# Kernel optimization log

Measured on AMD Instinct MI355X. Metric: run time of the kernel, lower is better.

The kernel has to match this reference:

```python
import jax, jax.numpy as jnp
import numpy as np

B, N, M, C1, C2 = 4, 8192, 2048, 128, 256
H1, H2 = 256, 128  # mlp = [C2+C1, 256, 128]
EPS_DIST = 1e-8
EPS_BN = 1e-5
K = 3


def setup_inputs() -> dict:
    key = jax.random.key(0)
    ks = jax.random.split(key, 6)
    return {
        "unknown": jax.random.normal(ks[0], (B, N, 3), dtype=jnp.float32),
        "known": jax.random.normal(ks[1], (B, M, 3), dtype=jnp.float32),
        "unknow_feats": jax.random.normal(ks[2], (B, C1, N), dtype=jnp.float32),
        "known_feats": jax.random.normal(ks[3], (B, C2, M), dtype=jnp.float32),
        "W1": jax.random.normal(ks[4], (H1, C1 + C2), dtype=jnp.float32) * 0.05,
        "g1": jnp.ones((H1,), jnp.float32),
        "b1": jnp.zeros((H1,), jnp.float32),
        "W2": jax.random.normal(ks[5], (H2, H1), dtype=jnp.float32) * 0.05,
        "g2": jnp.ones((H2,), jnp.float32),
        "b2": jnp.zeros((H2,), jnp.float32),
    }


def _bn_relu(x, g, b):
    # training-mode BatchNorm over (batch, spatial) axes for (B, C, N) tensor
    mean = jnp.mean(x, axis=(0, 2), keepdims=True)
    var = jnp.var(x, axis=(0, 2), keepdims=True)
    y = (x - mean) * jax.lax.rsqrt(var + EPS_BN) * g[None, :, None] + b[None, :, None]
    return jax.nn.relu(y)


def reference(unknown, known, unknow_feats, known_feats, W1, g1, b1, W2, g2, b2):
    # 3-NN: squared euclidean distances (B, N, M) via expansion (avoids B,N,M,3 temp)
    d2 = (
        jnp.sum(unknown * unknown, axis=-1)[:, :, None]
        + jnp.sum(known * known, axis=-1)[:, None, :]
        - 2.0 * jnp.einsum("bnc,bmc->bnm", unknown, known)
    )
    neg_d, idx = jax.lax.top_k(-d2, K)  # smallest-K squared dists
    dist = -neg_d  # (B, N, K), squared distances (pytorch3d knn_points convention)
    recip = 1.0 / (dist + EPS_DIST)
    weight = recip / jnp.sum(recip, axis=2, keepdims=True)  # (B, N, K)

    kf = jnp.swapaxes(known_feats, 1, 2)  # (B, M, C2)
    grouped = jax.vmap(lambda f, i: f[i])(kf, idx)  # (B, N, K, C2)
    interp = jnp.einsum("bnkc,bnk->bcn", grouped, weight)  # (B, C2, N)

    x = jnp.concatenate([interp, unknow_feats], axis=1)  # (B, C2+C1, N)
    x = _bn_relu(jnp.einsum("oc,bcn->bon", W1, x), g1, b1)
    x = _bn_relu(jnp.einsum("oc,bcn->bon", W2, x), g2, b2)
    return x  # (B, H2, N)
```

## Files before the change

### kernel.cpp

```cpp
#include <hip/hip_runtime.h>
#include <hip/hip_bf16.h>
#include <cstdint>
#include <cstddef>

typedef unsigned short u16;
typedef __attribute__((ext_vector_type(8))) short bf16x8;
typedef __attribute__((ext_vector_type(4))) float f32x4;

constexpr int Bn = 4;
constexpr int Nq = 8192;
constexpr int Mk = 2048;
constexpr int C1c = 128;
constexpr int C2c = 256;
constexpr int H1c = 256;
constexpr int H2c = 128;

__device__ __forceinline__ float bf2f(u16 u) {
    union { uint32_t i; float f; } v;
    v.i = (uint32_t)u << 16;
    return v.f;
}
__device__ __forceinline__ u16 f2bf(float f) {
    const uint32_t x = __float_as_uint(f);
    return (u16)((x + 0x7FFFu + ((x >> 16) & 1u)) >> 16);
}
__device__ __forceinline__ uint32_t cvtpk(float lo, float hi) {
    uint32_t r;
    asm("v_cvt_pk_bf16_f32 %0, %1, %2" : "=v"(r) : "v"(lo), "v"(hi));
    return r;
}

__global__ __launch_bounds__(256) void knn_prep_kernel(
    const float* __restrict__ W1, const float* __restrict__ W2,
    u16* __restrict__ W1b, u16* __restrict__ W2b,
    const float* __restrict__ KF, u16* __restrict__ Ptb,
    const float* __restrict__ UF, u16* __restrict__ UFt,
    const float* __restrict__ unknown, const float* __restrict__ known,
    int* __restrict__ idx_out, float* __restrict__ w_out)
{
    __shared__ __align__(16) char smem[32768];
    const int bid = blockIdx.x;
    const int t = threadIdx.x;

    if (bid < 1024) {
        float4* kp = (float4*)smem;
        const int b = bid >> 8;
        const int n0 = (bid & 255) * 32;

        const float* kb = known + (size_t)b * Mk * 3;
        for (int i = t; i < Mk; i += 256) {
            const float x = kb[i * 3 + 0], y = kb[i * 3 + 1], z = kb[i * 3 + 2];
            kp[i] = make_float4(x, y, z, fmaf(x, x, fmaf(y, y, z * z)));
        }
        __syncthreads();

        const int q = n0 + (t >> 3);
        const int s = t & 7;
        const float* u = unknown + ((size_t)b * Nq + q) * 3;
        const float ux = u[0], uy = u[1], uz = u[2];
        const float nux = -2.0f * ux, nuy = -2.0f * uy, nuz = -2.0f * uz;
        const float uu = fmaf(ux, ux, fmaf(uy, uy, uz * uz));

        float d0 = 1e30f, d1 = 1e30f, d2 = 1e30f;
        int i0 = 0, i1 = 0, i2 = 0;

        auto ins = [&](float d, int i) {
            const bool c0 = d < d0, c1 = d < d1, c2 = d < d2;
            const float nd0 = fminf(d0, d);
            const float nd1 = __builtin_amdgcn_fmed3f(d0, d, d1);
            const float nd2 = __builtin_amdgcn_fmed3f(d1, d, d2);
            i2 = c1 ? i1 : (c2 ? i : i2);
            i1 = c0 ? i0 : (c1 ? i : i1);
            i0 = c0 ? i : i0;
            d0 = nd0; d1 = nd1; d2 = nd2;
        };

        #pragma unroll 8
        for (int it = 0; it < Mk / 8; ++it) {
            const int m = it * 8 + s;
            const float4 p = kp[m];
            const float d = fmaf(nux, p.x, fmaf(nuy, p.y, fmaf(nuz, p.z, p.w)));
            ins(d, m);
        }
        #pragma unroll
        for (int off = 1; off <= 4; off <<= 1) {
            const float e0 = __shfl_xor(d0, off), e1 = __shfl_xor(d1, off), e2 = __shfl_xor(d2, off);
            const int j0 = __shfl_xor(i0, off), j1 = __shfl_xor(i1, off), j2 = __shfl_xor(i2, off);
            ins(e0, j0);
            ins(e1, j1);
            ins(e2, j2);
        }
        if (s == 0) {
            const float f0 = d0 + uu, f1 = d1 + uu, f2 = d2 + uu;
            const float r0 = 1.0f / (f0 + 1e-8f);
            const float r1 = 1.0f / (f1 + 1e-8f);
            const float r2 = 1.0f / (f2 + 1e-8f);
            const float inv = 1.0f / (r0 + r1 + r2);
            const size_t base = ((size_t)b * Nq + q) * 3;
            idx_out[base + 0] = i0;
            idx_out[base + 1] = i1;
            idx_out[base + 2] = i2;
            w_out[base + 0] = r0 * inv;
            w_out[base + 1] = r1 * inv;
            w_out[base + 2] = r2 * inv;
        }
    } else if (bid < 1152) {
        const int cb = bid - 1024;
        const float* X = (cb < 96) ? W1 : W2;
        u16* Y = (cb < 96) ? W1b : W2b;
        const int i = ((cb < 96) ? cb : (cb - 96)) * 256 + t;
        const float4 v = *(const float4*)&X[(size_t)i * 4];
        ushort4 o;
        o.x = f2bf(v.x); o.y = f2bf(v.y); o.z = f2bf(v.z); o.w = f2bf(v.w);
        *(ushort4*)&Y[(size_t)i * 4] = o;
    } else if (bid < 1664) {
        u16* As = (u16*)smem;
        u16* Bs = (u16*)(smem + 5120);
        const int f = bid - 1152;
        const int b = f >> 7;
        const int rem = f & 127;
        const int m0 = (rem >> 2) * 64;
        const int h0 = (rem & 3) * 64;
        const float* KFb = KF + (size_t)b * C2c * Mk;
        const int l = t & 63, wv = t >> 6;
        const int wr = wv >> 1, wc = wv & 1;

        f32x4 acc[2][2];
        const f32x4 z = {0.0f, 0.0f, 0.0f, 0.0f};
        acc[0][0] = z; acc[0][1] = z; acc[1][0] = z; acc[1][1] = z;

        const int cA = t >> 3;
        const int mcA = (t & 7) * 8;
        const int hB = t >> 2;
        const int khB = (t & 3) * 8;

        for (int kt = 0; kt < 8; ++kt) {
            const int kc = kt * 32;
            {
                const float* src = &KFb[(size_t)(kc + cA) * Mk + m0 + mcA];
                const float4 v0 = *(const float4*)&src[0];
                const float4 v1 = *(const float4*)&src[4];
                As[(mcA + 0) * 40 + cA] = f2bf(v0.x);
                As[(mcA + 1) * 40 + cA] = f2bf(v0.y);
                As[(mcA + 2) * 40 + cA] = f2bf(v0.z);
                As[(mcA + 3) * 40 + cA] = f2bf(v0.w);
                As[(mcA + 4) * 40 + cA] = f2bf(v1.x);
                As[(mcA + 5) * 40 + cA] = f2bf(v1.y);
                As[(mcA + 6) * 40 + cA] = f2bf(v1.z);
                As[(mcA + 7) * 40 + cA] = f2bf(v1.w);
            }
            {
                const float* src = &W1[(size_t)(h0 + hB) * 384 + kc + khB];
                const float4 v0 = *(const float4*)&src[0];
                const float4 v1 = *(const float4*)&src[4];
                u16 o[8] = {f2bf(v0.x), f2bf(v0.y), f2bf(v0.z), f2bf(v0.w),
                            f2bf(v1.x), f2bf(v1.y), f2bf(v1.z), f2bf(v1.w)};
                *(uint4*)&Bs[hB * 40 + khB] = *(const uint4*)o;
            }
            __syncthreads();
            bf16x8 af[2], bf[2];
            #pragma unroll
            for (int ff = 0; ff < 2; ++ff) {
                af[ff] = *(const bf16x8*)&As[(wr * 32 + ff * 16 + (l & 15)) * 40 + (l >> 4) * 8];
                bf[ff] = *(const bf16x8*)&Bs[(wc * 32 + ff * 16 + (l & 15)) * 40 + (l >> 4) * 8];
            }
            #pragma unroll
            for (int i = 0; i < 2; ++i)
                #pragma unroll
                for (int j = 0; j < 2; ++j)
                    acc[i][j] = __builtin_amdgcn_mfma_f32_16x16x32_bf16(af[i], bf[j], acc[i][j], 0, 0, 0);
            __syncthreads();
        }

        u16* Pb = Ptb + (size_t)b * Mk * 256;
        const int cb = l & 15, rg = (l >> 4) * 4;
        #pragma unroll
        for (int i = 0; i < 2; ++i) {
            #pragma unroll
            for (int r = 0; r < 4; ++r) {
                const int row = m0 + wr * 32 + i * 16 + rg + r;
                #pragma unroll
                for (int j = 0; j < 2; ++j)
                    Pb[(size_t)row * 256 + h0 + wc * 32 + j * 16 + cb] = f2bf(acc[i][j][r]);
            }
        }
    } else {
        const int f = bid - 1664;
        const int b = f >> 8, rem = f & 255;
        const int m0 = (rem >> 1) * 64, c0 = (rem & 1) * 64;
        const float* X = UF + (size_t)b * C1c * Nq;
        u16* Y = UFt + (size_t)b * Nq * C1c;
        float (*T)[65] = (float(*)[65])smem;
        const int m4 = (t & 15) * 4, cr = t >> 4;
        #pragma unroll
        for (int i = 0; i < 4; ++i) {
            const float4 v = *(const float4*)&X[(size_t)(c0 + cr + i * 16) * Nq + m0 + m4];
            T[cr + i * 16][m4 + 0] = v.x;
            T[cr + i * 16][m4 + 1] = v.y;
            T[cr + i * 16][m4 + 2] = v.z;
            T[cr + i * 16][m4 + 3] = v.w;
        }
        __syncthreads();
        const int c4 = (t & 15) * 4, mr = t >> 4;
        #pragma unroll
        for (int i = 0; i < 4; ++i) {
            const int m = mr + i * 16;
            ushort4 o;
            o.x = f2bf(T[c4 + 0][m]);
            o.y = f2bf(T[c4 + 1][m]);
            o.z = f2bf(T[c4 + 2][m]);
            o.w = f2bf(T[c4 + 3][m]);
            *(ushort4*)&Y[(size_t)(m0 + m) * C1c + c0 + c4] = o;
        }
    }
}

__global__ __launch_bounds__(256) void mfma_gemm2(
    const u16* __restrict__ A,
    const u16* __restrict__ Bt,
    u16* __restrict__ Cout,
    const u16* __restrict__ Ptb,
    const int* __restrict__ idx, const float* __restrict__ wgt,
    float* __restrict__ partS, float* __restrict__ partQ)
{
    __shared__ __align__(16) char smem[16384];
    __shared__ float redS[4][128], redQ[4][128];
    u16* As = (u16*)smem;
    u16* Bs = (u16*)(smem + 8192);
    float (*Ytmp)[128] = (float(*)[128])smem;

    const int b = blockIdx.z;
    const int m0 = blockIdx.x * 128, n0 = blockIdx.y * 128;
    const int t = threadIdx.x;
    const int l = t & 63, wv = t >> 6;
    const int wr = wv >> 1, wc = wv & 1;

    const u16* Ab = A + (size_t)b * Nq * C1c;
    const int rA0 = t >> 2, rA1 = (t + 256) >> 2;
    const int ko = (t & 3) * 8;

    f32x4 acc[4][4];
    const f32x4 z = {0.0f, 0.0f, 0.0f, 0.0f};
    #pragma unroll
    for (int i = 0; i < 4; ++i)
        #pragma unroll
        for (int j = 0; j < 4; ++j) acc[i][j] = z;

    uint4 a0 = *(const uint4*)&Ab[(size_t)(m0 + rA0) * C1c + ko];
    uint4 a1 = *(const uint4*)&Ab[(size_t)(m0 + rA1) * C1c + ko];
    uint4 b0 = *(const uint4*)&Bt[(size_t)(n0 + rA0) * 384 + ko];
    uint4 b1 = *(const uint4*)&Bt[(size_t)(n0 + rA1) * 384 + ko];

    for (int kt = 0; kt < C1c / 32; ++kt) {
        *(uint4*)&As[t * 8] = a0;
        *(uint4*)&As[(t + 256) * 8] = a1;
        *(uint4*)&Bs[t * 8] = b0;
        *(uint4*)&Bs[(t + 256) * 8] = b1;
        __syncthreads();
        if (kt + 1 < C1c / 32) {
            const int k0 = (kt + 1) * 32;
            a0 = *(const uint4*)&Ab[(size_t)(m0 + rA0) * C1c + k0 + ko];
            a1 = *(const uint4*)&Ab[(size_t)(m0 + rA1) * C1c + k0 + ko];
            b0 = *(const uint4*)&Bt[(size_t)(n0 + rA0) * 384 + k0 + ko];
            b1 = *(const uint4*)&Bt[(size_t)(n0 + rA1) * 384 + k0 + ko];
        }
        bf16x8 af[4], bf[4];
        #pragma unroll
        for (int f = 0; f < 4; ++f) {
            af[f] = *(const bf16x8*)&As[(wr * 64 + f * 16 + (l & 15)) * 32 + (l >> 4) * 8];
            bf[f] = *(const bf16x8*)&Bs[(wc * 64 + f * 16 + (l & 15)) * 32 + (l >> 4) * 8];
        }
        #pragma unroll
        for (int i = 0; i < 4; ++i)
            #pragma unroll
            for (int j = 0; j < 4; ++j)
                acc[i][j] = __builtin_amdgcn_mfma_f32_16x16x32_bf16(af[i], bf[j], acc[i][j], 0, 0, 0);
        __syncthreads();
    }

    const int cb = l & 15;
    const int rg = (l >> 4) * 4;
    const int colblk = t & 15;
    const int rowblk = t >> 4;
    float s8[8] = {0, 0, 0, 0, 0, 0, 0, 0}, q8[8] = {0, 0, 0, 0, 0, 0, 0, 0};
    const u16* Pb = Ptb + (size_t)b * Mk * 256;

    for (int q = 0; q < 4; ++q) {
        __syncthreads();
        if (wr == (q >> 1)) {
            #pragma unroll
            for (int ii = 0; ii < 2; ++ii) {
                const int i = (q & 1) * 2 + ii;
                #pragma unroll
                for (int r = 0; r < 4; ++r) {
                    const int Rq = ii * 16 + rg + r;
                    #pragma unroll
                    for (int j = 0; j < 4; ++j)
                        Ytmp[Rq][wc * 64 + j * 16 + cb] = acc[i][j][r];
                }
            }
        }
        __syncthreads();
        #pragma unroll
        for (int rr = 0; rr < 2; ++rr) {
            const int Rq = rowblk * 2 + rr;
            const int R = m0 + q * 32 + Rq;
            const size_t ib = ((size_t)b * Nq + R) * 3;
            const int j0 = idx[ib], j1 = idx[ib + 1], j2 = idx[ib + 2];
            const float w0 = wgt[ib], w1 = wgt[ib + 1], w2 = wgt[ib + 2];
            const int c8 = colblk * 8;
            const int Cc0 = n0 + c8;
            const float* yrow = &Ytmp[Rq][c8];
            const float4 y0 = *(const float4*)&yrow[0];
            const float4 y1v = *(const float4*)&yrow[4];
            const uint4 p0 = *(const uint4*)&Pb[(size_t)j0 * 256 + Cc0];
            const uint4 p1 = *(const uint4*)&Pb[(size_t)j1 * 256 + Cc0];
            const uint4 p2 = *(const uint4*)&Pb[(size_t)j2 * 256 + Cc0];
            const u16* pp0 = (const u16*)&p0;
            const u16* pp1 = (const u16*)&p1;
            const u16* pp2 = (const u16*)&p2;
            const float* ya = (const float*)&y0;
            const float* yb = (const float*)&y1v;
            float v[8];
            #pragma unroll
            for (int c = 0; c < 8; ++c) {
                const float a = (c < 4) ? ya[c] : yb[c - 4];
                const float vv = a + w0 * bf2f(pp0[c]) + w1 * bf2f(pp1[c]) + w2 * bf2f(pp2[c]);
                v[c] = vv;
                s8[c] += vv;
                q8[c] += vv * vv;
            }
            uint4 o;
            uint32_t* po = (uint32_t*)&o;
            po[0] = cvtpk(v[0], v[1]);
            po[1] = cvtpk(v[2], v[3]);
            po[2] = cvtpk(v[4], v[5]);
            po[3] = cvtpk(v[6], v[7]);
            *(uint4*)&Cout[(size_t)b * Nq * 256 + (size_t)R * 256 + Cc0] = o;
        }
    }

    #pragma unroll
    for (int c = 0; c < 8; ++c) {
        s8[c] += __shfl_xor(s8[c], 16);
        s8[c] += __shfl_xor(s8[c], 32);
        q8[c] += __shfl_xor(q8[c], 16);
        q8[c] += __shfl_xor(q8[c], 32);
    }
    if (l < 16) {
        #pragma unroll
        for (int c = 0; c < 8; ++c) {
            redS[wv][l * 8 + c] = s8[c];
            redQ[wv][l * 8 + c] = q8[c];
        }
    }
    __syncthreads();
    if (t < 128) {
        const float S = redS[0][t] + redS[1][t] + redS[2][t] + redS[3][t];
        const float Q = redQ[0][t] + redQ[1][t] + redQ[2][t] + redQ[3][t];
        const int pblk = blockIdx.z * gridDim.x + blockIdx.x;
        partS[(size_t)pblk * 256 + blockIdx.y * 128 + t] = S;
        partQ[(size_t)pblk * 256 + blockIdx.y * 128 + t] = Q;
    }
}

__global__ __launch_bounds__(256) void bn1_finalize_mb(
    const float* __restrict__ pS, const float* __restrict__ pQ,
    const float* __restrict__ g, const float* __restrict__ beta,
    float* __restrict__ scale, float* __restrict__ bias)
{
    __shared__ float rs[256], rq[256];
    const int cc = threadIdx.x & 15;
    const int sl = threadIdx.x >> 4;
    const int ch = blockIdx.x * 16 + cc;
    float s = 0.0f, q = 0.0f;
    for (int i = sl; i < 256; i += 16) {
        s += pS[(size_t)i * 256 + ch];
        q += pQ[(size_t)i * 256 + ch];
    }
    rs[threadIdx.x] = s;
    rq[threadIdx.x] = q;
    __syncthreads();
    if (sl == 0) {
        for (int k = 1; k < 16; ++k) {
            s += rs[k * 16 + cc];
            q += rq[k * 16 + cc];
        }
        const float cnt = (float)(Bn * Nq);
        const float mean = s / cnt;
        const float var = q / cnt - mean * mean;
        const float rv = rsqrtf(var + 1e-5f);
        const float sc = g[ch] * rv;
        scale[ch] = sc;
        bias[ch] = beta[ch] - mean * sc;
    }
}

__device__ __forceinline__ uint4 bnx(uint4 x, const float* scs, const float* bis, int k) {
    const u16* p = (const u16*)&x;
    const float4 s0 = *(const float4*)&scs[k];
    const float4 s1 = *(const float4*)&scs[k + 4];
    const float4 b0 = *(const float4*)&bis[k];
    const float4 b1 = *(const float4*)&bis[k + 4];
    const float* sa = (const float*)&s0;
    const float* sb = (const float*)&s1;
    const float* ba = (const float*)&b0;
    const float* bb = (const float*)&b1;
    uint4 o;
    uint32_t* po = (uint32_t*)&o;
    #pragma unroll
    for (int w2 = 0; w2 < 2; ++w2) {
        const float a0 = fmaxf(0.0f, fmaf(bf2f(p[2 * w2 + 0]), sa[2 * w2 + 0], ba[2 * w2 + 0]));
        const float a1 = fmaxf(0.0f, fmaf(bf2f(p[2 * w2 + 1]), sa[2 * w2 + 1], ba[2 * w2 + 1]));
        po[w2] = cvtpk(a0, a1);
    }
    #pragma unroll
    for (int w2 = 0; w2 < 2; ++w2) {
        const float a0 = fmaxf(0.0f, fmaf(bf2f(p[4 + 2 * w2 + 0]), sb[2 * w2 + 0], bb[2 * w2 + 0]));
        const float a1 = fmaxf(0.0f, fmaf(bf2f(p[4 + 2 * w2 + 1]), sb[2 * w2 + 1], bb[2 * w2 + 1]));
        po[2 + w2] = cvtpk(a0, a1);
    }
    return o;
}

__global__ __launch_bounds__(256) void mfma_gemm3(
    const u16* __restrict__ W2b,
    const u16* __restrict__ Y,
    float* __restrict__ out,
    const float* __restrict__ bn_s, const float* __restrict__ bn_b,
    float* __restrict__ partS, float* __restrict__ partQ)
{
    __shared__ u16 As[2048];
    __shared__ u16 Bs[4096];
    __shared__ float scs[256], bis[256];
    __shared__ float sS[2][64], sQ[2][64];

    const int b = blockIdx.z;
    const int m0 = blockIdx.x * 64;
    const int n0 = blockIdx.y * 128;
    const int t = threadIdx.x;
    const int l = t & 63, wv = t >> 6;
    const int wr = wv >> 1, wc = wv & 1;

    scs[t] = bn_s[t];
    bis[t] = bn_b[t];

    const u16* Yb = Y + (size_t)b * Nq * 256;
    const int rA = t >> 2;
    const int rB1 = (t + 256) >> 2;
    const int ko = (t & 3) * 8;

    f32x4 acc[2][4];
    const f32x4 z = {0.0f, 0.0f, 0.0f, 0.0f};
    #pragma unroll
    for (int i = 0; i < 2; ++i)
        #pragma unroll
        for (int j = 0; j < 4; ++j) acc[i][j] = z;

    uint4 a0 = *(const uint4*)&W2b[(size_t)(m0 + rA) * 256 + ko];
    uint4 b0 = *(const uint4*)&Yb[(size_t)(n0 + rA) * 256 + ko];
    uint4 b1 = *(const uint4*)&Yb[(size_t)(n0 + rB1) * 256 + ko];
    __syncthreads();

    for (int kt = 0; kt < 8; ++kt) {
        const int k = kt * 32 + ko;
        *(uint4*)&As[t * 8] = a0;
        *(uint4*)&Bs[t * 8] = bnx(b0, scs, bis, k);
        *(uint4*)&Bs[(t + 256) * 8] = bnx(b1, scs, bis, k);
        __syncthreads();
        if (kt + 1 < 8) {
            const int k0 = (kt + 1) * 32;
            a0 = *(const uint4*)&W2b[(size_t)(m0 + rA) * 256 + k0 + ko];
            b0 = *(const uint4*)&Yb[(size_t)(n0 + rA) * 256 + k0 + ko];
            b1 = *(const uint4*)&Yb[(size_t)(n0 + rB1) * 256 + k0 + ko];
        }
        bf16x8 af[2], bf[4];
        #pragma unroll
        for (int f = 0; f < 2; ++f)
            af[f] = *(const bf16x8*)&As[(wr * 32 + f * 16 + (l & 15)) * 32 + (l >> 4) * 8];
        #pragma unroll
        for (int f = 0; f < 4; ++f)
            bf[f] = *(const bf16x8*)&Bs[(wc * 64 + f * 16 + (l & 15)) * 32 + (l >> 4) * 8];
        #pragma unroll
        for (int i = 0; i < 2; ++i)
            #pragma unroll
            for (int j = 0; j < 4; ++j)
                acc[i][j] = __builtin_amdgcn_mfma_f32_16x16x32_bf16(af[i], bf[j], acc[i][j], 0, 0, 0);
        __syncthreads();
    }

    const int cb = l & 15;
    const int rg = (l >> 4) * 4;
    float* ob = out + (size_t)b * H2c * Nq;
    #pragma unroll
    for (int i = 0; i < 2; ++i) {
        #pragma unroll
        for (int r = 0; r < 4; ++r) {
            const int Rl = wr * 32 + i * 16 + rg + r;
            #pragma unroll
            for (int j = 0; j < 4; ++j) {
                const int Cc = n0 + wc * 64 + j * 16 + cb;
                ob[(size_t)(m0 + Rl) * Nq + Cc] = acc[i][j][r];
            }
            float s = acc[i][0][r] + acc[i][1][r] + acc[i][2][r] + acc[i][3][r];
            float q = acc[i][0][r] * acc[i][0][r] + acc[i][1][r] * acc[i][1][r] +
                      acc[i][2][r] * acc[i][2][r] + acc[i][3][r] * acc[i][3][r];
            s += __shfl_xor(s, 1); s += __shfl_xor(s, 2);
            s += __shfl_xor(s, 4); s += __shfl_xor(s, 8);
            q += __shfl_xor(q, 1); q += __shfl_xor(q, 2);
            q += __shfl_xor(q, 4); q += __shfl_xor(q, 8);
            if ((l & 15) == 0) {
                sS[wc][Rl] = s;
                sQ[wc][Rl] = q;
            }
        }
    }
    __syncthreads();
    if (t < 64) {
        const float S = sS[0][t] + sS[1][t];
        const float Q = sQ[0][t] + sQ[1][t];
        const int p = blockIdx.z * gridDim.y + blockIdx.y;
        partS[(size_t)p * 128 + m0 + t] = S;
        partQ[(size_t)p * 128 + m0 + t] = Q;
    }
}

__global__ __launch_bounds__(256) void bn2_apply_kernel(
    float* __restrict__ Y,
    const float* __restrict__ pS, const float* __restrict__ pQ,
    const float* __restrict__ g, const float* __restrict__ beta)
{
    __shared__ float rs[256], rq[256];
    const int t = threadIdx.x;
    const size_t base = (size_t)blockIdx.x * 1024;
    const int c = (int)((base / Nq) % H2c);

    rs[t] = pS[(size_t)t * 128 + c];
    rq[t] = pQ[(size_t)t * 128 + c];
    __syncthreads();
    for (int off = 128; off > 0; off >>= 1) {
        if (t < off) {
            rs[t] += rs[t + off];
            rq[t] += rq[t + off];
        }
        __syncthreads();
    }
    if (t == 0) {
        const float cnt = (float)(Bn * Nq);
        const float mean = rs[0] / cnt;
        const float var = rq[0] / cnt - mean * mean;
        const float r = rsqrtf(var + 1e-5f);
        const float sc = g[c] * r;
        rs[0] = sc;
        rq[0] = beta[c] - mean * sc;
    }
    __syncthreads();
    const float sc = rs[0], bi = rq[0];
    float4 v = *(float4*)&Y[base + t * 4];
    v.x = fmaxf(0.0f, fmaf(v.x, sc, bi));
    v.y = fmaxf(0.0f, fmaf(v.y, sc, bi));
    v.z = fmaxf(0.0f, fmaf(v.z, sc, bi));
    v.w = fmaxf(0.0f, fmaf(v.w, sc, bi));
    *(float4*)&Y[base + t * 4] = v;
}

extern "C" void kernel_launch(void* const* d_in, const int* in_sizes, int n_in,
                              void* d_out, int out_size, void* d_ws, size_t ws_size,
                              hipStream_t stream) {
    const float* unknown = (const float*)d_in[0];
    const float* known = (const float*)d_in[1];
    const float* unknow_feats = (const float*)d_in[2];
    const float* known_feats = (const float*)d_in[3];
    const float* W1 = (const float*)d_in[4];
    const float* g1 = (const float*)d_in[5];
    const float* b1 = (const float*)d_in[6];
    const float* W2 = (const float*)d_in[7];
    const float* g2 = (const float*)d_in[8];
    const float* b2 = (const float*)d_in[9];
    float* out = (float*)d_out;

    char* w = (char*)d_ws;
    u16* UFt = (u16*)w; w += (size_t)Bn * Nq * C1c * 2;
    u16* W1b = (u16*)w; w += (size_t)H1c * 384 * 2;
    u16* W2b = (u16*)w; w += (size_t)H2c * H1c * 2;
    u16* Ptb = (u16*)w; w += (size_t)Bn * Mk * H1c * 2;
    u16* y1b = (u16*)w; w += (size_t)Bn * Nq * H1c * 2;
    int* idx = (int*)w; w += (size_t)Bn * Nq * 3 * 4;
    float* wgt = (float*)w; w += (size_t)Bn * Nq * 3 * 4;
    float* pS1 = (float*)w; w += (size_t)256 * 256 * 4;
    float* pQ1 = (float*)w; w += (size_t)256 * 256 * 4;
    float* pS2 = (float*)w; w += (size_t)256 * 128 * 4;
    float* pQ2 = (float*)w; w += (size_t)256 * 128 * 4;
    float* scale1 = (float*)w; w += 1024;
    float* bias1 = (float*)w; w += 1024;

    knn_prep_kernel<<<2688, 256, 0, stream>>>(W1, W2, W1b, W2b,
                                              known_feats, Ptb, unknow_feats, UFt,
                                              unknown, known, idx, wgt);

    mfma_gemm2<<<dim3(Nq / 128, H1c / 128, Bn), 256, 0, stream>>>(
        UFt, W1b + C2c, y1b, Ptb, idx, wgt, pS1, pQ1);

    bn1_finalize_mb<<<16, 256, 0, stream>>>(pS1, pQ1, g1, b1, scale1, bias1);

    mfma_gemm3<<<dim3(2, Nq / 128, Bn), 256, 0, stream>>>(
        W2b, y1b, out, scale1, bias1, pS2, pQ2);

    bn2_apply_kernel<<<(Bn * H2c * Nq) / 1024, 256, 0, stream>>>(out, pS2, pQ2, g2, b2);
}
```

Before: 92.68 us.

## Store GEMM3 output as bf16 and split BN2 into finalize and apply kernels

GEMM3 now writes its pre-normalization output as bf16 into a workspace buffer instead of fp32 into the output. A small new kernel reduces the per-block partial sums once per channel into scale and bias. The apply kernel then reads bf16 and writes fp32, eliminating the per-block redundant 256-way reduction and the fp32 read. This adds one kernel launch and loses precision in the intermediate before normalization.

```diff
diff --git a/kernel.cpp b/kernel.cpp
--- a/kernel.cpp
+++ b/kernel.cpp
@@ -216,10 +216,8 @@
 }
 
 __global__ __launch_bounds__(256) void mfma_gemm2(
-    const u16* __restrict__ A,
-    const u16* __restrict__ Bt,
-    u16* __restrict__ Cout,
-    const u16* __restrict__ Ptb,
+    const u16* __restrict__ A, const u16* __restrict__ Bt,
+    u16* __restrict__ Cout, const u16* __restrict__ Ptb,
     const int* __restrict__ idx, const float* __restrict__ wgt,
     float* __restrict__ partS, float* __restrict__ partQ)
 {
@@ -426,7 +424,7 @@
 __global__ __launch_bounds__(256) void mfma_gemm3(
     const u16* __restrict__ W2b,
     const u16* __restrict__ Y,
-    float* __restrict__ out,
+    u16* __restrict__ y2b,
     const float* __restrict__ bn_s, const float* __restrict__ bn_b,
     float* __restrict__ partS, float* __restrict__ partQ)
 {
@@ -491,7 +489,7 @@
 
     const int cb = l & 15;
     const int rg = (l >> 4) * 4;
-    float* ob = out + (size_t)b * H2c * Nq;
+    u16* ob = y2b + (size_t)b * H2c * Nq;
     #pragma unroll
     for (int i = 0; i < 2; ++i) {
         #pragma unroll
@@ -500,7 +498,7 @@
             #pragma unroll
             for (int j = 0; j < 4; ++j) {
                 const int Cc = n0 + wc * 64 + j * 16 + cb;
-                ob[(size_t)(m0 + Rl) * Nq + Cc] = acc[i][j][r];
+                ob[(size_t)(m0 + Rl) * Nq + Cc] = f2bf(acc[i][j][r]);
             }
             float s = acc[i][0][r] + acc[i][1][r] + acc[i][2][r] + acc[i][3][r];
             float q = acc[i][0][r] * acc[i][0][r] + acc[i][1][r] * acc[i][1][r] +
@@ -525,43 +523,59 @@
     }
 }
 
-__global__ __launch_bounds__(256) void bn2_apply_kernel(
-    float* __restrict__ Y,
+__global__ __launch_bounds__(256) void bn2_finalize_mb(
     const float* __restrict__ pS, const float* __restrict__ pQ,
-    const float* __restrict__ g, const float* __restrict__ beta)
+    const float* __restrict__ g, const float* __restrict__ beta,
+    float* __restrict__ scale, float* __restrict__ bias)
 {
     __shared__ float rs[256], rq[256];
-    const int t = threadIdx.x;
-    const size_t base = (size_t)blockIdx.x * 1024;
+    const int cc = threadIdx.x & 15;
+    const int sl = threadIdx.x >> 4;
+    const int ch = blockIdx.x * 16 + cc;
+    float s = 0.0f, q = 0.0f;
+    for (int i = sl; i < 256; i += 16) {
+        s += pS[(size_t)i * 128 + ch];
+        q += pQ[(size_t)i * 128 + ch];
+    }
+    rs[threadIdx.x] = s;
+    rq[threadIdx.x] = q;
+    __syncthreads();
+    if (sl == 0) {
+        for (int k = 1; k < 16; ++k) {
+            s += rs[k * 16 + cc];
+            q += rq[k * 16 + cc];
+        }
+        const float cnt = (float)(Bn * Nq);
+        const float mean = s / cnt;
+        const float var = q / cnt - mean * mean;
+        const float rv = rsqrtf(var + 1e-5f);
+        const float sc = g[ch] * rv;
+        scale[ch] = sc;
+        bias[ch] = beta[ch] - mean * sc;
+    }
+}
+
+__global__ __launch_bounds__(256) void bn2_apply_simple(
+    const u16* __restrict__ y2b, float* __restrict__ out,
+    const float* __restrict__ scale, const float* __restrict__ bias)
+{
+    const size_t base = (size_t)blockIdx.x * 2048;
     const int c = (int)((base / Nq) % H2c);
-
-    rs[t] = pS[(size_t)t * 128 + c];
-    rq[t] = pQ[(size_t)t * 128 + c];
-    __syncthreads();
-    for (int off = 128; off > 0; off >>= 1) {
-        if (t < off) {
-            rs[t] += rs[t + off];
-            rq[t] += rq[t + off];
-        }
-        __syncthreads();
-    }
-    if (t == 0) {
-        const float cnt = (float)(Bn * Nq);
-        const float mean = rs[0] / cnt;
-        const float var = rq[0] / cnt - mean * mean;
-        const float r = rsqrtf(var + 1e-5f);
-        const float sc = g[c] * r;
-        rs[0] = sc;
-        rq[0] = beta[c] - mean * sc;
-    }
-    __syncthreads();
-    const float sc = rs[0], bi = rq[0];
-    float4 v = *(float4*)&Y[base + t * 4];
-    v.x = fmaxf(0.0f, fmaf(v.x, sc, bi));
-    v.y = fmaxf(0.0f, fmaf(v.y, sc, bi));
-    v.z = fmaxf(0.0f, fmaf(v.z, sc, bi));
-    v.w = fmaxf(0.0f, fmaf(v.w, sc, bi));
-    *(float4*)&Y[base + t * 4] = v;
+    const float sc = scale[c], bi = bias[c];
+    const size_t i = base + threadIdx.x * 8;
+    const uint4 v = *(const uint4*)&y2b[i];
+    const u16* pv = (const u16*)&v;
+    float4 o0, o1;
+    o0.x = fmaxf(0.0f, fmaf(bf2f(pv[0]), sc, bi));
+    o0.y = fmaxf(0.0f, fmaf(bf2f(pv[1]), sc, bi));
+    o0.z = fmaxf(0.0f, fmaf(bf2f(pv[2]), sc, bi));
+    o0.w = fmaxf(0.0f, fmaf(bf2f(pv[3]), sc, bi));
+    o1.x = fmaxf(0.0f, fmaf(bf2f(pv[4]), sc, bi));
+    o1.y = fmaxf(0.0f, fmaf(bf2f(pv[5]), sc, bi));
+    o1.z = fmaxf(0.0f, fmaf(bf2f(pv[6]), sc, bi));
+    o1.w = fmaxf(0.0f, fmaf(bf2f(pv[7]), sc, bi));
+    *(float4*)&out[i] = o0;
+    *(float4*)&out[i + 4] = o1;
 }
 
 extern "C" void kernel_launch(void* const* d_in, const int* in_sizes, int n_in,
@@ -585,6 +599,7 @@
     u16* W2b = (u16*)w; w += (size_t)H2c * H1c * 2;
     u16* Ptb = (u16*)w; w += (size_t)Bn * Mk * H1c * 2;
     u16* y1b = (u16*)w; w += (size_t)Bn * Nq * H1c * 2;
+    u16* y2b = (u16*)w; w += (size_t)Bn * H2c * Nq * 2;
     int* idx = (int*)w; w += (size_t)Bn * Nq * 3 * 4;
     float* wgt = (float*)w; w += (size_t)Bn * Nq * 3 * 4;
     float* pS1 = (float*)w; w += (size_t)256 * 256 * 4;
@@ -593,6 +608,8 @@
     float* pQ2 = (float*)w; w += (size_t)256 * 128 * 4;
     float* scale1 = (float*)w; w += 1024;
     float* bias1 = (float*)w; w += 1024;
+    float* scale2 = (float*)w; w += 1024;
+    float* bias2 = (float*)w; w += 1024;
 
     knn_prep_kernel<<<2688, 256, 0, stream>>>(W1, W2, W1b, W2b,
                                               known_feats, Ptb, unknow_feats, UFt,
@@ -604,7 +621,9 @@
     bn1_finalize_mb<<<16, 256, 0, stream>>>(pS1, pQ1, g1, b1, scale1, bias1);
 
     mfma_gemm3<<<dim3(2, Nq / 128, Bn), 256, 0, stream>>>(
-        W2b, y1b, out, scale1, bias1, pS2, pQ2);
-
-    bn2_apply_kernel<<<(Bn * H2c * Nq) / 1024, 256, 0, stream>>>(out, pS2, pQ2, g2, b2);
-}
+        W2b, y1b, y2b, scale1, bias1, pS2, pQ2);
+
+    bn2_finalize_mb<<<8, 256, 0, stream>>>(pS2, pQ2, g2, b2, scale2, bias2);
+
+    bn2_apply_simple<<<(Bn * H2c * Nq) / 2048, 256, 0, stream>>>(y2b, out, scale2, bias2);
+}
```

After: 91.24 us. Within noise of the previous version (-1.6%).
